# Kernel optimization log

Measured on AMD Instinct MI355X. Metric: run time of the kernel, lower is better.

Reference implementation:

```python
import jax, jax.numpy as jnp
import numpy as np

N, G, H1, H2, HEADS, EMB, C, S = 4096, 2048, 512, 128, 8, 16, 20, 4
CH = H1 // HEADS  # per-head channels = 64
EPS = 1e-6
COEF_FE = 0.1


def _uni(k, shape, fan_in, fan_out):
    c = np.sqrt(6.0 / (fan_in + fan_out)).astype(np.float32)
    return jax.random.uniform(k, shape, jnp.float32, -c, c)


def setup_inputs() -> dict:
    key = jax.random.key(0)
    ks = jax.random.split(key, 40)
    adj = (jax.random.uniform(ks[0], (N, N)) < 0.005).astype(jnp.float32)
    adj = jnp.maximum(adj, jnp.eye(N, dtype=jnp.float32))  # self-loops, no empty rows
    node_feats = jax.random.normal(ks[1], (N, G), jnp.float32)
    count_matrix = jax.random.randint(ks[2], (N, G), 0, 50).astype(jnp.float32)
    library_size = jax.random.uniform(ks[3], (N, 1), jnp.float32, 0.5, 2.0)
    slice_label = jax.random.randint(ks[4], (N,), 0, S)
    basis = jax.random.uniform(ks[5], (C, G), jnp.float32)
    # encoder GAT layer1: HEADS heads, c_in=G -> c_out=CH each
    We1 = _uni(ks[6], (HEADS, CH, G), G, CH)
    be1 = jnp.zeros((HEADS, CH), jnp.float32)
    v0e1 = _uni(ks[7], (HEADS, CH, 1), CH, 1)
    v1e1 = _uni(ks[8], (HEADS, CH, 1), CH, 1)
    # encoder dense layer2: H1 -> H2
    W2 = _uni(ks[9], (H2, H1), H1, H2)
    b2 = jnp.zeros((H2,), jnp.float32)
    # decoder GAT layer1: c_in = H2+EMB -> CH per head
    CIN_D = H2 + EMB
    Wd1 = _uni(ks[10], (HEADS, CH, CIN_D), CIN_D, CH)
    bd1 = jnp.zeros((HEADS, CH), jnp.float32)
    v0d1 = _uni(ks[11], (HEADS, CH, 1), CH, 1)
    v1d1 = _uni(ks[12], (HEADS, CH, 1), CH, 1)
    # decoder dense layer2: H1 -> G
    Wd2 = _uni(ks[13], (G, H1), H1, G)
    bd2 = jnp.zeros((G,), jnp.float32)
    # deconv alpha (H2+EMB -> 1) and beta (H2 -> C); zero-init in torch, small random here
    Wa = 0.01 * jax.random.normal(ks[14], (1, CIN_D), jnp.float32)
    ba = jnp.zeros((1,), jnp.float32)
    Wb = 0.01 * jax.random.normal(ks[15], (C, H2), jnp.float32)
    bb = jnp.zeros((C,), jnp.float32)
    gamma = 0.01 * jax.random.normal(ks[16], (S, G), jnp.float32)
    logtheta = 5.0 * jnp.ones((S, G), jnp.float32)
    emb_table = jax.random.normal(ks[17], (S, EMB), jnp.float32)
    return dict(adj_matrix=adj, node_feats=node_feats, count_matrix=count_matrix,
                library_size=library_size, slice_label=slice_label, basis=basis,
                We1=We1, be1=be1, v0e1=v0e1, v1e1=v1e1, W2=W2, b2=b2,
                Wd1=Wd1, bd1=bd1, v0d1=v0d1, v1d1=v1d1, Wd2=Wd2, bd2=bd2,
                Wa=Wa, ba=ba, Wb=Wb, bb=bb, gamma=gamma, logtheta=logtheta,
                emb_table=emb_table)


def _gat_head(x, adj, W, b, v0, v1):
    h = x @ W.T + b                       # [N, CH]
    logits = adj * ((h @ v0) + (h @ v1).T)  # [N, N]; zero where adj==0
    s = jax.nn.sigmoid(logits) - 0.5       # unnormalized attentions
    mask = adj != 0.0
    e = jnp.where(mask, jnp.exp(s), 0.0)    # sparse softmax over structural nonzeros (temp=1)
    den = e.sum(axis=1, keepdims=True)
    p = e / jnp.where(den == 0.0, 1.0, den)
    return p @ h                            # [N, CH]


def _gat_multi(x, adj, Ws, bs, v0s, v1s):
    return jnp.concatenate([_gat_head(x, adj, Ws[i], bs[i], v0s[i], v1s[i])
                            for i in range(HEADS)], axis=1)


def reference(adj_matrix, node_feats, count_matrix, library_size, slice_label, basis,
              We1, be1, v0e1, v1e1, W2, b2, Wd1, bd1, v0d1, v1d1, Wd2, bd2,
              Wa, ba, Wb, bb, gamma, logtheta, emb_table):
    # encoder
    H = jax.nn.elu(_gat_multi(node_feats, adj_matrix, We1, be1, v0e1, v1e1))
    Z = H @ W2.T + b2                                   # [N, H2]
    emb = emb_table[slice_label]                        # [N, EMB]
    # deconvolutioner
    beta = jax.nn.softmax(jax.nn.elu(Z) @ Wb.T + bb, axis=1)   # [N, C]
    Hc = jax.nn.elu(jnp.concatenate([Z, emb], axis=1))
    alpha = Hc @ Wa.T + ba                              # [N, 1]
    # decoder
    Hd = jax.nn.elu(_gat_multi(jnp.concatenate([Z, emb], axis=1), adj_matrix,
                               Wd1, bd1, v0d1, v1d1))
    X_recon = Hd @ Wd2.T + bd2                          # [N, G]
    features_loss = jnp.mean(jnp.sqrt(jnp.sum((node_feats - X_recon) ** 2, axis=1)))
    # NB deconvolution loss
    log_lam = jnp.log(beta @ basis + EPS) + alpha + gamma[slice_label]
    lam = jnp.exp(log_lam)
    th = jnp.exp(logtheta)[slice_label]                 # [N, G]
    mu = library_size * lam
    ll = (jax.lax.lgamma(count_matrix + th + EPS) - jax.lax.lgamma(th + EPS)
          + th * jnp.log(th + EPS) - th * jnp.log(th + mu + EPS)
          + count_matrix * jnp.log(mu + EPS) - count_matrix * jnp.log(th + mu + EPS))
    decon_loss = -jnp.mean(jnp.sum(ll, axis=1))
    return decon_loss + COEF_FE * features_loss
```

## Files before the change

### kernel.cpp

```cpp
#include <hip/hip_runtime.h>
#include <hip/hip_bf16.h>
#include <math.h>

#define N 4096
#define G 2048
#define H1 512
#define H2 128
#define HEADS 8
#define EMB 16
#define C 20
#define S 4
#define CH 64
#define CIN_D (H2 + EMB)
#define KD_PAD 160
#define KB_PAD 32
#define CAP 128
#define EPSV 1e-6f

typedef __attribute__((ext_vector_type(8))) short short8;
typedef __attribute__((ext_vector_type(8))) short bf16x8;
typedef __attribute__((ext_vector_type(4))) float f32x4;

__device__ __forceinline__ unsigned short f2b(float x) {
    __hip_bfloat16 h = __float2bfloat16(x);
    return *reinterpret_cast<unsigned short*>(&h);
}
__device__ __forceinline__ float b2f(unsigned short u) {
    unsigned int x = ((unsigned int)u) << 16;
    return __uint_as_float(x);
}
__device__ __forceinline__ float lgamma_fast(float x) {
    float sh = 0.f;
    while (x < 8.f) { sh -= __logf(x); x += 1.f; }
    float ix = 1.f / x;
    float lx = __logf(x);
    return (x - 0.5f) * lx - x + 0.91893853f
         + ix * (0.08333333f - 0.00277778f * ix * ix) + sh;
}

__global__ void build_csr(const float* __restrict__ adj, int* __restrict__ col_idx,
                          int* __restrict__ row_cnt) {
    int i = blockIdx.x;
    int lane = threadIdx.x;
    int cnt = 0;
    const float4* row4 = (const float4*)(adj + (size_t)i * N);
    int* cols = col_idx + (size_t)i * CAP;
    unsigned long long lmask = (1ull << lane) - 1ull;
    for (int c = 0; c < N / 256; ++c) {
        float4 v = row4[c * 64 + lane];
        float vv[4] = {v.x, v.y, v.z, v.w};
        #pragma unroll
        for (int s = 0; s < 4; ++s) {
            unsigned long long m = __ballot(vv[s] != 0.f);
            if (vv[s] != 0.f) {
                int idx = cnt + __popcll(m & lmask);
                if (idx < CAP) cols[idx] = c * 256 + lane * 4 + s;
            }
            cnt += __popcll(m);
        }
    }
    if (lane == 0) row_cnt[i] = cnt < CAP ? cnt : CAP;
}

#define SEG_SG   (S * G)
#define SEG_NF4  (N * G / 4)
#define SEG_WE4  (H1 * G / 4)
#define SEG_W24  (H2 * H1 / 4)
#define SEG_WD1E (H1 * KD_PAD)
#define SEG_WD24 (G * H1 / 4)
#define SEG_BTE  (G * KB_PAD)
#define PREP_TOTAL (SEG_SG + SEG_NF4 + SEG_WE4 + SEG_W24 + SEG_WD1E + SEG_WD24 + SEG_BTE)

__device__ __forceinline__ void cvt4(const float* __restrict__ in,
                                     unsigned short* __restrict__ out, int i) {
    float4 v = ((const float4*)in)[i];
    ushort4 o;
    o.x = f2b(v.x); o.y = f2b(v.y); o.z = f2b(v.z); o.w = f2b(v.w);
    ((ushort4*)out)[i] = o;
}

__global__ __launch_bounds__(256) void prep(const float* __restrict__ logtheta,
                                            const float* __restrict__ gamma,
                                            float* __restrict__ th_a, float* __restrict__ eg_a,
                                            float* __restrict__ gm_a, float* __restrict__ ax_a,
                                            const float* __restrict__ node_f,
                                            unsigned short* __restrict__ nf_bf,
                                            const float* __restrict__ We1,
                                            unsigned short* __restrict__ We1_bf,
                                            const float* __restrict__ W2,
                                            unsigned short* __restrict__ W2_bf,
                                            const float* __restrict__ Wd1,
                                            unsigned short* __restrict__ Wd1_bf,
                                            const float* __restrict__ Wd2,
                                            unsigned short* __restrict__ Wd2_bf,
                                            const float* __restrict__ basis,
                                            unsigned short* __restrict__ basisT_bf) {
    int idx = blockIdx.x * 256 + threadIdx.x;
    if (idx < SEG_SG) {
        float th = __expf(logtheta[idx]);
        float gm = gamma[idx];
        th_a[idx] = th;
        eg_a[idx] = __expf(gm);
        gm_a[idx] = gm;
        ax_a[idx] = th * __logf(th + EPSV) - lgammaf(th + EPSV);
        return;
    }
    idx -= SEG_SG;
    if (idx < SEG_NF4) { cvt4(node_f, nf_bf, idx); return; }
    idx -= SEG_NF4;
    if (idx < SEG_WE4) { cvt4(We1, We1_bf, idx); return; }
    idx -= SEG_WE4;
    if (idx < SEG_W24) { cvt4(W2, W2_bf, idx); return; }
    idx -= SEG_W24;
    if (idx < SEG_WD1E) {
        int n = idx / KD_PAD, k = idx - n * KD_PAD;
        Wd1_bf[idx] = f2b(k < CIN_D ? Wd1[n * CIN_D + k] : 0.f);
        return;
    }
    idx -= SEG_WD1E;
    if (idx < SEG_WD24) { cvt4(Wd2, Wd2_bf, idx); return; }
    idx -= SEG_WD24;
    if (idx < SEG_BTE) {
        int g = idx >> 5, c = idx & 31;
        basisT_bf[idx] = f2b(c < C ? basis[c * G + g] : 0.f);
    }
}

#define LDP 40
template<int FM, int OBF, int KS, int HV>
__global__ __launch_bounds__(256) void gemm_mfma(const unsigned short* __restrict__ A,
                                                 const unsigned short* __restrict__ B,
                                                 const float* __restrict__ bias,
                                                 void* __restrict__ Cout,
                                                 int M, int Nc, int K,
                                                 const float* __restrict__ v0f,
                                                 const float* __restrict__ v1f,
                                                 float* __restrict__ hv0,
                                                 float* __restrict__ hv1) {
    constexpr int BMT = FM * 32;
    __shared__ short As[BMT * LDP];
    __shared__ short Bs[128 * LDP];
    int bn = blockIdx.x, bm = blockIdx.y;
    int kz = (KS > 1) ? blockIdx.z : 0;
    int t = threadIdx.x;
    int lane = t & 63, wid = t >> 6;
    int wr = wid >> 1, wc = wid & 1;
    f32x4 acc[FM][4] = {};
    const short* Ag = (const short*)A + (size_t)(bm * BMT) * K;
    const short* Bg = (const short*)B + (size_t)(bn * 128) * K;
    int r0 = t >> 2, q0 = t & 3;
    int rbase = (lane & 15);
    int koff = (lane >> 4) * 8;
    int kbeg = kz * (K / KS), kend = kbeg + K / KS;

    for (int k0 = kbeg; k0 < kend; k0 += 32) {
        short8 a0 = *(const short8*)(Ag + (size_t)r0 * K + k0 + q0 * 8);
        short8 a1;
        if constexpr (FM == 4) a1 = *(const short8*)(Ag + (size_t)(r0 + 64) * K + k0 + q0 * 8);
        short8 b0 = *(const short8*)(Bg + (size_t)r0 * K + k0 + q0 * 8);
        short8 b1 = *(const short8*)(Bg + (size_t)(r0 + 64) * K + k0 + q0 * 8);
        __syncthreads();
        *(short8*)(As + r0 * LDP + q0 * 8) = a0;
        if constexpr (FM == 4) *(short8*)(As + (r0 + 64) * LDP + q0 * 8) = a1;
        *(short8*)(Bs + r0 * LDP + q0 * 8) = b0;
        *(short8*)(Bs + (r0 + 64) * LDP + q0 * 8) = b1;
        __syncthreads();
        bf16x8 af[FM], bfr[4];
        #pragma unroll
        for (int m = 0; m < FM; ++m)
            af[m] = *(const bf16x8*)(As + (wr * FM * 16 + m * 16 + rbase) * LDP + koff);
        #pragma unroll
        for (int n = 0; n < 4; ++n)
            bfr[n] = *(const bf16x8*)(Bs + (wc * 64 + n * 16 + rbase) * LDP + koff);
        #pragma unroll
        for (int m = 0; m < FM; ++m)
            #pragma unroll
            for (int n = 0; n < 4; ++n)
                acc[m][n] = __builtin_amdgcn_mfma_f32_16x16x32_bf16(af[m], bfr[n], acc[m][n], 0, 0, 0);
    }
    int colb = bn * 128 + wc * 64;
    int rowb = bm * BMT + wr * FM * 16;
    #pragma unroll
    for (int m = 0; m < FM; ++m) {
        #pragma unroll
        for (int n = 0; n < 4; ++n) {
            int col = colb + n * 16 + (lane & 15);
            int row0 = rowb + m * 16 + (lane >> 4) * 4;
            if constexpr (KS > 1) {
                float* Cp = (float*)Cout + (size_t)kz * M * Nc;
                #pragma unroll
                for (int r = 0; r < 4; ++r)
                    Cp[(size_t)(row0 + r) * Nc + col] = acc[m][n][r];
            } else {
                float bs = bias ? bias[col] : 0.f;
                #pragma unroll
                for (int r = 0; r < 4; ++r) {
                    float v = acc[m][n][r] + bs;
                    if constexpr (OBF)
                        ((unsigned short*)Cout)[(size_t)(row0 + r) * Nc + col] = f2b(v);
                    else
                        ((float*)Cout)[(size_t)(row0 + r) * Nc + col] = v;
                }
            }
        }
    }
    if constexpr (HV) {
        int h = colb >> 6;
        #pragma unroll
        for (int m = 0; m < FM; ++m) {
            #pragma unroll
            for (int r = 0; r < 4; ++r) {
                int row = rowb + m * 16 + (lane >> 4) * 4 + r;
                float p0 = 0.f, p1 = 0.f;
                #pragma unroll
                for (int n = 0; n < 4; ++n) {
                    int col = colb + n * 16 + (lane & 15);
                    float v = acc[m][n][r] + bias[col];
                    p0 += v * v0f[col];
                    p1 += v * v1f[col];
                }
                p0 += __shfl_xor(p0, 1); p0 += __shfl_xor(p0, 2);
                p0 += __shfl_xor(p0, 4); p0 += __shfl_xor(p0, 8);
                p1 += __shfl_xor(p1, 1); p1 += __shfl_xor(p1, 2);
                p1 += __shfl_xor(p1, 4); p1 += __shfl_xor(p1, 8);
                if ((lane & 15) == 0) {
                    hv0[row * HEADS + h] = p0;
                    hv1[row * HEADS + h] = p1;
                }
            }
        }
    }
}

template<int KS>
__global__ __launch_bounds__(256) void reduce_k(const float* __restrict__ Cp,
                                                const float* __restrict__ bias,
                                                float* __restrict__ out,
                                                int total4, int ncmask) {
    int i = blockIdx.x * 256 + threadIdx.x;
    if (i >= total4) return;
    float4 s = ((const float4*)Cp)[i];
    #pragma unroll
    for (int ks = 1; ks < KS; ++ks) {
        float4 v = ((const float4*)(Cp + (size_t)ks * total4 * 4))[i];
        s.x += v.x; s.y += v.y; s.z += v.z; s.w += v.w;
    }
    int col = (i * 4) & ncmask;
    s.x += bias[col]; s.y += bias[col + 1]; s.z += bias[col + 2]; s.w += bias[col + 3];
    ((float4*)out)[i] = s;
}

template<int KS>
__global__ __launch_bounds__(256) void reduce_k_hv(const float* __restrict__ Cp,
                                                   const float* __restrict__ bias,
                                                   unsigned short* __restrict__ out,
                                                   const float* __restrict__ v0f,
                                                   const float* __restrict__ v1f,
                                                   float* __restrict__ hv0,
                                                   float* __restrict__ hv1) {
    constexpr int total4 = N * H1 / 4;
    int t = threadIdx.x;
    int i = blockIdx.x * 256 + t;
    float4 s = ((const float4*)Cp)[i];
    #pragma unroll
    for (int ks = 1; ks < KS; ++ks) {
        float4 v = ((const float4*)(Cp + (size_t)ks * total4 * 4))[i];
        s.x += v.x; s.y += v.y; s.z += v.z; s.w += v.w;
    }
    int col = (i * 4) & (H1 - 1);
    s.x += bias[col]; s.y += bias[col + 1]; s.z += bias[col + 2]; s.w += bias[col + 3];
    ushort4 o;
    o.x = f2b(s.x); o.y = f2b(s.y); o.z = f2b(s.z); o.w = f2b(s.w);
    ((ushort4*)out)[i] = o;
    int row = (i * 4) >> 9;
    int h = col >> 6;
    float4 w0 = *(const float4*)(v0f + col);
    float4 w1 = *(const float4*)(v1f + col);
    float p0 = s.x * w0.x + s.y * w0.y + s.z * w0.z + s.w * w0.w;
    float p1 = s.x * w1.x + s.y * w1.y + s.z * w1.z + s.w * w1.w;
    p0 += __shfl_xor(p0, 1); p0 += __shfl_xor(p0, 2);
    p0 += __shfl_xor(p0, 4); p0 += __shfl_xor(p0, 8);
    p1 += __shfl_xor(p1, 1); p1 += __shfl_xor(p1, 2);
    p1 += __shfl_xor(p1, 4); p1 += __shfl_xor(p1, 8);
    if ((t & 15) == 0) {
        hv0[row * HEADS + h] = p0;
        hv1[row * HEADS + h] = p1;
    }
}

__global__ __launch_bounds__(256) void gemm_recon_sq(const unsigned short* __restrict__ A,
                                                     const unsigned short* __restrict__ B,
                                                     const float* __restrict__ bias,
                                                     const unsigned short* __restrict__ nfb,
                                                     float* __restrict__ sq_part) {
    constexpr int K = H1;
    __shared__ short As[64 * LDP];
    __shared__ short Bs[128 * LDP];
    __shared__ float red[4][32];
    int bn = blockIdx.x, bm = blockIdx.y;
    int t = threadIdx.x;
    int lane = t & 63, wid = t >> 6;
    int wr = wid >> 1, wc = wid & 1;
    f32x4 acc[2][4] = {};
    const short* Ag = (const short*)A + (size_t)(bm * 64) * K;
    const short* Bg = (const short*)B + (size_t)(bn * 128) * K;
    int r0 = t >> 2, q0 = t & 3;
    int rbase = (lane & 15);
    int koff = (lane >> 4) * 8;

    for (int k0 = 0; k0 < K; k0 += 32) {
        short8 a0 = *(const short8*)(Ag + (size_t)r0 * K + k0 + q0 * 8);
        short8 b0 = *(const short8*)(Bg + (size_t)r0 * K + k0 + q0 * 8);
        short8 b1 = *(const short8*)(Bg + (size_t)(r0 + 64) * K + k0 + q0 * 8);
        __syncthreads();
        *(short8*)(As + r0 * LDP + q0 * 8) = a0;
        *(short8*)(Bs + r0 * LDP + q0 * 8) = b0;
        *(short8*)(Bs + (r0 + 64) * LDP + q0 * 8) = b1;
        __syncthreads();
        bf16x8 af[2], bfr[4];
        #pragma unroll
        for (int m = 0; m < 2; ++m)
            af[m] = *(const bf16x8*)(As + (wr * 32 + m * 16 + rbase) * LDP + koff);
        #pragma unroll
        for (int n = 0; n < 4; ++n)
            bfr[n] = *(const bf16x8*)(Bs + (wc * 64 + n * 16 + rbase) * LDP + koff);
        #pragma unroll
        for (int m = 0; m < 2; ++m)
            #pragma unroll
            for (int n = 0; n < 4; ++n)
                acc[m][n] = __builtin_amdgcn_mfma_f32_16x16x32_bf16(af[m], bfr[n], acc[m][n], 0, 0, 0);
    }
    int colb = bn * 128 + wc * 64;
    int rowb = bm * 64 + wr * 32;
    float part[2][4];
    #pragma unroll
    for (int m = 0; m < 2; ++m) {
        #pragma unroll
        for (int r = 0; r < 4; ++r) part[m][r] = 0.f;
        #pragma unroll
        for (int n = 0; n < 4; ++n) {
            int col = colb + n * 16 + (lane & 15);
            float bs = bias[col];
            int row0 = rowb + m * 16 + (lane >> 4) * 4;
            #pragma unroll
            for (int r = 0; r < 4; ++r) {
                float d = b2f(nfb[(size_t)(row0 + r) * G + col]) - (acc[m][n][r] + bs);
                part[m][r] += d * d;
            }
        }
    }
    #pragma unroll
    for (int m = 0; m < 2; ++m)
        #pragma unroll
        for (int r = 0; r < 4; ++r) {
            float v = part[m][r];
            v += __shfl_xor(v, 1); v += __shfl_xor(v, 2);
            v += __shfl_xor(v, 4); v += __shfl_xor(v, 8);
            part[m][r] = v;
        }
    if ((lane & 15) == 0) {
        int q = lane >> 4;
        #pragma unroll
        for (int m = 0; m < 2; ++m)
            #pragma unroll
            for (int r = 0; r < 4; ++r)
                red[wid][m * 16 + q * 4 + r] = part[m][r];
    }
    __syncthreads();
    if (t < 64) {
        int wr2 = t >> 5, loc = t & 31;
        float v = red[wr2 * 2 + 0][loc] + red[wr2 * 2 + 1][loc];
        sq_part[(size_t)(bm * 64 + t) * 16 + bn] = v;
    }
}

__global__ __launch_bounds__(256) void bd_ll(const unsigned short* __restrict__ A,
                                             const unsigned short* __restrict__ B,
                                             const float* __restrict__ cm,
                                             const int* __restrict__ slab,
                                             const float* __restrict__ muf,
                                             const float* __restrict__ kco,
                                             const float* __restrict__ th_a,
                                             const float* __restrict__ eg_a,
                                             const float* __restrict__ gm_a,
                                             const float* __restrict__ ax_a,
                                             float* __restrict__ ll_part) {
    __shared__ short As[32 * LDP];
    __shared__ short Bs[128 * LDP];
    __shared__ float red[4][16];
    int bn = blockIdx.x, bm = blockIdx.y;
    int t = threadIdx.x;
    int lane = t & 63, wid = t >> 6;
    int wr = wid >> 1, wc = wid & 1;
    f32x4 acc[4] = {};
    const short* Ag = (const short*)A + (size_t)(bm * 32) * KB_PAD;
    const short* Bg = (const short*)B + (size_t)(bn * 128) * KB_PAD;
    int r0 = t >> 2, q0 = t & 3;
    if (t < 128) {
        short8 a0 = *(const short8*)(Ag + (size_t)r0 * KB_PAD + q0 * 8);
        *(short8*)(As + r0 * LDP + q0 * 8) = a0;
    }
    {
        short8 b0 = *(const short8*)(Bg + (size_t)r0 * KB_PAD + q0 * 8);
        short8 b1 = *(const short8*)(Bg + (size_t)(r0 + 64) * KB_PAD + q0 * 8);
        *(short8*)(Bs + r0 * LDP + q0 * 8) = b0;
        *(short8*)(Bs + (r0 + 64) * LDP + q0 * 8) = b1;
    }
    __syncthreads();
    int rbase = (lane & 15);
    int koff = (lane >> 4) * 8;
    bf16x8 af = *(const bf16x8*)(As + (wr * 16 + rbase) * LDP + koff);
    bf16x8 bfr[4];
    #pragma unroll
    for (int n = 0; n < 4; ++n)
        bfr[n] = *(const bf16x8*)(Bs + (wc * 64 + n * 16 + rbase) * LDP + koff);
    #pragma unroll
    for (int n = 0; n < 4; ++n)
        acc[n] = __builtin_amdgcn_mfma_f32_16x16x32_bf16(af, bfr[n], acc[n], 0, 0, 0);
    int colb = bn * 128 + wc * 64;
    int rowb = bm * 32 + wr * 16;
    #pragma unroll
    for (int r = 0; r < 4; ++r) {
        int row = rowb + (lane >> 4) * 4 + r;
        int sl = slab[row];
        float mufv = muf[row], kcov = kco[row];
        size_t sgb = (size_t)sl * G;
        float p = 0.f;
        #pragma unroll
        for (int n = 0; n < 4; ++n) {
            int col = colb + n * 16 + (lane & 15);
            float ebd = acc[n][r] + EPSV;
            float k = cm[(size_t)row * G + col];
            float th = th_a[sgb + col];
            float lbd = __logf(ebd);
            float mu = mufv * ebd * eg_a[sgb + col];
            float lgx = lgamma_fast(k + th + EPSV);
            p += lgx + ax_a[sgb + col] - (th + k) * __logf(th + mu + EPSV)
               + k * (kcov + lbd + gm_a[sgb + col]);
        }
        p += __shfl_xor(p, 1); p += __shfl_xor(p, 2);
        p += __shfl_xor(p, 4); p += __shfl_xor(p, 8);
        if ((lane & 15) == 0) red[wid][(lane >> 4) * 4 + r] = p;
    }
    __syncthreads();
    if (t < 32) {
        int wr2 = t >> 4, rl = t & 15;
        float v = red[wr2 * 2 + 0][rl] + red[wr2 * 2 + 1][rl];
        ll_part[(size_t)(bm * 32 + wr2 * 16 + rl) * 16 + bn] = v;
    }
}

__global__ __launch_bounds__(512) void attn_fused(const unsigned short* __restrict__ Hb,
                                                  const float* __restrict__ hv0,
                                                  const float* __restrict__ hv1,
                                                  const int* __restrict__ col_idx,
                                                  const int* __restrict__ row_cnt,
                                                  unsigned short* __restrict__ out) {
    __shared__ int scols[CAP];
    __shared__ float sw[CAP][HEADS];
    __shared__ float sden[HEADS];
    __shared__ float red[8][64 * 8];
    int i = blockIdx.x;
    int t = threadIdx.x;
    int cnt = row_cnt[i];
    const int* cols = col_idx + (size_t)i * CAP;
    if (t < cnt) scols[t] = cols[t];
    __syncthreads();
    for (int idx = t; idx < cnt * HEADS; idx += 512) {
        int e = idx >> 3, h = idx & 7;
        int j = scols[e];
        float x = hv0[i * HEADS + h] + hv1[j * HEADS + h];
        sw[e][h] = __expf(1.f / (1.f + __expf(-x)) - 0.5f);
    }
    __syncthreads();
    if (t < HEADS) {
        float d = 0.f;
        for (int e = 0; e < cnt; ++e) d += sw[e][t];
        sden[t] = 1.f / d;
    }
    __syncthreads();
    int slot = t >> 6;
    int cg = t & 63;
    int h = cg >> 3;
    float inv = sden[h];
    float acc[8];
    #pragma unroll
    for (int k = 0; k < 8; ++k) acc[k] = 0.f;
    for (int e = slot; e < cnt; e += 8) {
        int j = scols[e];
        float wv = sw[e][h] * inv;
        short8 hv = ((const short8*)(Hb + (size_t)j * H1))[cg];
        #pragma unroll
        for (int k = 0; k < 8; ++k)
            acc[k] += wv * b2f((unsigned short)hv[k]);
    }
    #pragma unroll
    for (int k = 0; k < 8; ++k) red[slot][cg * 8 + k] = acc[k];
    __syncthreads();
    if (slot < 4) {
        #pragma unroll
        for (int k = 0; k < 8; ++k) red[slot][cg * 8 + k] += red[slot + 4][cg * 8 + k];
    }
    __syncthreads();
    if (slot < 2) {
        #pragma unroll
        for (int k = 0; k < 8; ++k) red[slot][cg * 8 + k] += red[slot + 2][cg * 8 + k];
    }
    __syncthreads();
    if (slot == 0) {
        short8 o;
        #pragma unroll
        for (int k = 0; k < 8; ++k) {
            float v = red[0][cg * 8 + k] + red[1][cg * 8 + k];
            v = (v > 0.f) ? v : expm1f(v);
            o[k] = (short)f2b(v);
        }
        ((short8*)(out + (size_t)i * H1))[cg] = o;
    }
}

__global__ void pernode(const float* __restrict__ Z, const float* __restrict__ emb_table,
                        const int* __restrict__ slab, const float* __restrict__ Wb,
                        const float* __restrict__ bb, const float* __restrict__ Wa,
                        const float* __restrict__ ba, const float* __restrict__ lib,
                        unsigned short* __restrict__ beta_bf, float* __restrict__ muf,
                        float* __restrict__ kco, unsigned short* __restrict__ Xdb) {
    int i = blockIdx.x;
    int lane = threadIdx.x;
    __shared__ float sZ[H2];
    __shared__ float sE[EMB];
    __shared__ float sLog[C];
    __shared__ float sAl;
    sZ[lane] = Z[(size_t)i * H2 + lane];
    sZ[64 + lane] = Z[(size_t)i * H2 + 64 + lane];
    int s = slab[i];
    if (lane < EMB) sE[lane] = emb_table[s * EMB + lane];
    __syncthreads();
    Xdb[(size_t)i * KD_PAD + lane] = f2b(sZ[lane]);
    Xdb[(size_t)i * KD_PAD + 64 + lane] = f2b(sZ[64 + lane]);
    if (lane < EMB) Xdb[(size_t)i * KD_PAD + H2 + lane] = f2b(sE[lane]);
    if (lane < KD_PAD - CIN_D) Xdb[(size_t)i * KD_PAD + CIN_D + lane] = 0;
    if (lane < C) {
        float acc = bb[lane];
        for (int k = 0; k < H2; ++k) {
            float z = sZ[k];
            float e = z > 0.f ? z : expm1f(z);
            acc += e * Wb[lane * H2 + k];
        }
        sLog[lane] = acc;
    }
    __syncthreads();
    if (lane == 0) {
        float mx = sLog[0];
        for (int c = 1; c < C; ++c) mx = fmaxf(mx, sLog[c]);
        float sm = 0.f;
        for (int c = 0; c < C; ++c) { float e = __expf(sLog[c] - mx); sLog[c] = e; sm += e; }
        for (int c = 0; c < C; ++c) sLog[c] /= sm;
    }
    __syncthreads();
    if (lane < KB_PAD) beta_bf[(size_t)i * KB_PAD + lane] = (lane < C) ? f2b(sLog[lane]) : 0;
    float x0 = sZ[lane];        x0 = x0 > 0.f ? x0 : expm1f(x0);
    float x1 = sZ[64 + lane];   x1 = x1 > 0.f ? x1 : expm1f(x1);
    float p = x0 * Wa[lane] + x1 * Wa[64 + lane];
    if (lane < EMB) {
        float x2 = sE[lane];    x2 = x2 > 0.f ? x2 : expm1f(x2);
        p += x2 * Wa[H2 + lane];
    }
    #pragma unroll
    for (int m = 32; m; m >>= 1) p += __shfl_xor(p, m);
    if (lane == 0) sAl = p + ba[0];
    __syncthreads();
    if (lane == 0) {
        float A = sAl, L = lib[i];
        muf[i] = L * __expf(A);
        kco[i] = __logf(L) + A;
    }
}

__global__ void row_reduce(const float* __restrict__ ll_part, const float* __restrict__ sq_part,
                           float* __restrict__ part_ll, float* __restrict__ part_sq) {
    int blk = blockIdx.x, lane = threadIdx.x;
    int row = blk * 64 + lane;
    float s1 = 0.f, s2 = 0.f;
    #pragma unroll
    for (int j = 0; j < 16; ++j) {
        s1 += ll_part[(size_t)row * 16 + j];
        s2 += sq_part[(size_t)row * 16 + j];
    }
    float b = sqrtf(s2);
    #pragma unroll
    for (int m = 32; m; m >>= 1) { s1 += __shfl_xor(s1, m); b += __shfl_xor(b, m); }
    if (lane == 0) { part_ll[blk] = s1; part_sq[blk] = b; }
}

__global__ void finalize2(const float* __restrict__ part_ll, const float* __restrict__ part_sq,
                          float* __restrict__ out) {
    int lane = threadIdx.x;
    float a = part_ll[lane], b = part_sq[lane];
    #pragma unroll
    for (int m = 32; m; m >>= 1) { a += __shfl_xor(a, m); b += __shfl_xor(b, m); }
    if (lane == 0) out[0] = -(a / (float)N) + 0.1f * (b / (float)N);
}

extern "C" void kernel_launch(void* const* d_in, const int* in_sizes, int n_in,
                              void* d_out, int out_size, void* d_ws, size_t ws_size,
                              hipStream_t stream) {
    const float* adj       = (const float*)d_in[0];
    const float* node_f    = (const float*)d_in[1];
    const float* count_m   = (const float*)d_in[2];
    const float* lib       = (const float*)d_in[3];
    const int*   slab      = (const int*)d_in[4];
    const float* basis     = (const float*)d_in[5];
    const float* We1       = (const float*)d_in[6];
    const float* be1       = (const float*)d_in[7];
    const float* v0e1      = (const float*)d_in[8];
    const float* v1e1      = (const float*)d_in[9];
    const float* W2        = (const float*)d_in[10];
    const float* b2        = (const float*)d_in[11];
    const float* Wd1       = (const float*)d_in[12];
    const float* bd1       = (const float*)d_in[13];
    const float* v0d1      = (const float*)d_in[14];
    const float* v1d1      = (const float*)d_in[15];
    const float* Wd2       = (const float*)d_in[16];
    const float* bd2       = (const float*)d_in[17];
    const float* Wa        = (const float*)d_in[18];
    const float* ba        = (const float*)d_in[19];
    const float* Wb        = (const float*)d_in[20];
    const float* bb        = (const float*)d_in[21];
    const float* gamma     = (const float*)d_in[22];
    const float* logtheta  = (const float*)d_in[23];
    const float* emb_table = (const float*)d_in[24];
    float* out = (float*)d_out;

    char* w = (char*)d_ws;
    auto alloc = [&](size_t bytes) { void* p = (void*)w; w += (bytes + 255) & ~(size_t)255; return p; };
    int*   col_idx = (int*)  alloc((size_t)N * CAP * 4);
    int*   row_cnt = (int*)  alloc((size_t)N * 4);
    unsigned short* Hlin_bf = (unsigned short*)alloc((size_t)N * H1 * 2);
    unsigned short* Hgat_bf = (unsigned short*)alloc((size_t)N * H1 * 2);
    float* Z       = (float*)alloc((size_t)N * H2 * 4);
    unsigned short* Xd_bf   = (unsigned short*)alloc((size_t)N * KD_PAD * 2);
    unsigned short* beta_bf = (unsigned short*)alloc((size_t)N * KB_PAD * 2);
    float* muf     = (float*)alloc((size_t)N * 4);
    float* kco     = (float*)alloc((size_t)N * 4);
    float* hv0     = (float*)alloc((size_t)N * HEADS * 4);
    float* hv1     = (float*)alloc((size_t)N * HEADS * 4);
    float* th_a    = (float*)alloc((size_t)S * G * 4);
    float* eg_a    = (float*)alloc((size_t)S * G * 4);
    float* gm_a    = (float*)alloc((size_t)S * G * 4);
    float* ax_a    = (float*)alloc((size_t)S * G * 4);
    float* Cp      = (float*)alloc((size_t)4 * N * H1 * 4);
    float* ll_part = (float*)alloc((size_t)N * 16 * 4);
    float* sq_part = (float*)alloc((size_t)N * 16 * 4);
    float* part_ll = (float*)alloc(64 * 4);
    float* part_sq = (float*)alloc(64 * 4);
    unsigned short* nf_bf    = (unsigned short*)alloc((size_t)N * G * 2);
    unsigned short* We1_bf   = (unsigned short*)alloc((size_t)H1 * G * 2);
    unsigned short* W2_bf    = (unsigned short*)alloc((size_t)H2 * H1 * 2);
    unsigned short* Wd1_bf   = (unsigned short*)alloc((size_t)H1 * KD_PAD * 2);
    unsigned short* Wd2_bf   = (unsigned short*)alloc((size_t)G * H1 * 2);
    unsigned short* basisT_bf= (unsigned short*)alloc((size_t)G * KB_PAD * 2);

    build_csr<<<dim3(N), dim3(64), 0, stream>>>(adj, col_idx, row_cnt);
    prep<<<dim3(PREP_TOTAL / 256), dim3(256), 0, stream>>>(
        logtheta, gamma, th_a, eg_a, gm_a, ax_a,
        node_f, nf_bf, We1, We1_bf, W2, W2_bf, Wd1, Wd1_bf, Wd2, Wd2_bf, basis, basisT_bf);

    gemm_mfma<2, 0, 4, 0><<<dim3(H1 / 128, N / 64, 4), dim3(256), 0, stream>>>(
        nf_bf, We1_bf, be1, Cp, N, H1, G, nullptr, nullptr, nullptr, nullptr);
    reduce_k_hv<4><<<dim3(N * H1 / 4 / 256), dim3(256), 0, stream>>>(
        Cp, be1, Hlin_bf, v0e1, v1e1, hv0, hv1);
    attn_fused<<<dim3(N), dim3(512), 0, stream>>>(Hlin_bf, hv0, hv1, col_idx, row_cnt, Hgat_bf);
    gemm_mfma<2, 0, 8, 0><<<dim3(H2 / 128, N / 64, 8), dim3(256), 0, stream>>>(
        Hgat_bf, W2_bf, b2, Cp, N, H2, H1, nullptr, nullptr, nullptr, nullptr);
    reduce_k<8><<<dim3((N * H2 / 4 + 255) / 256), dim3(256), 0, stream>>>(
        Cp, b2, Z, N * H2 / 4, H2 - 1);
    pernode<<<dim3(N), dim3(64), 0, stream>>>(Z, emb_table, slab, Wb, bb, Wa, ba, lib,
                                              beta_bf, muf, kco, Xd_bf);
    bd_ll<<<dim3(G / 128, N / 32), dim3(256), 0, stream>>>(
        beta_bf, basisT_bf, count_m, slab, muf, kco, th_a, eg_a, gm_a, ax_a, ll_part);
    gemm_mfma<2, 1, 1, 1><<<dim3(H1 / 128, N / 64), dim3(256), 0, stream>>>(
        Xd_bf, Wd1_bf, bd1, Hlin_bf, N, H1, KD_PAD, v0d1, v1d1, hv0, hv1);
    attn_fused<<<dim3(N), dim3(512), 0, stream>>>(Hlin_bf, hv0, hv1, col_idx, row_cnt, Hgat_bf);
    gemm_recon_sq<<<dim3(G / 128, N / 64), dim3(256), 0, stream>>>(
        Hgat_bf, Wd2_bf, bd2, nf_bf, sq_part);
    row_reduce<<<dim3(64), dim3(64), 0, stream>>>(ll_part, sq_part, part_ll, part_sq);
    finalize2<<<dim3(1), dim3(64), 0, stream>>>(part_ll, part_sq, out);
}
```

Before: 186.1 us.

## Split fused beta@basis GEMM and NB loss into GEMM plus row-wise elementwise kernel

Replaces the fused bd_ll kernel, which computed beta@basis via MFMA and evaluated the negative-binomial log-likelihood in the MFMA output layout, with two steps. The first is a generic gemm_mfma that writes beta@basis to a bf16 N×G buffer. The second is a row-per-wavefront elementwise kernel that reads it with vectorized coalesced loads and reduces each row directly. The aim is coalesced access to count_matrix and the per-slice tables and no cross-block partial sums. The cost is an extra 16 MB write and read of the intermediate and one more kernel launch.

```diff
diff --git a/kernel.cpp b/kernel.cpp
--- a/kernel.cpp
+++ b/kernel.cpp
@@ -374,80 +374,48 @@
     }
 }
 
-__global__ __launch_bounds__(256) void bd_ll(const unsigned short* __restrict__ A,
-                                             const unsigned short* __restrict__ B,
-                                             const float* __restrict__ cm,
-                                             const int* __restrict__ slab,
-                                             const float* __restrict__ muf,
-                                             const float* __restrict__ kco,
-                                             const float* __restrict__ th_a,
-                                             const float* __restrict__ eg_a,
-                                             const float* __restrict__ gm_a,
-                                             const float* __restrict__ ax_a,
-                                             float* __restrict__ ll_part) {
-    __shared__ short As[32 * LDP];
-    __shared__ short Bs[128 * LDP];
-    __shared__ float red[4][16];
-    int bn = blockIdx.x, bm = blockIdx.y;
-    int t = threadIdx.x;
-    int lane = t & 63, wid = t >> 6;
-    int wr = wid >> 1, wc = wid & 1;
-    f32x4 acc[4] = {};
-    const short* Ag = (const short*)A + (size_t)(bm * 32) * KB_PAD;
-    const short* Bg = (const short*)B + (size_t)(bn * 128) * KB_PAD;
-    int r0 = t >> 2, q0 = t & 3;
-    if (t < 128) {
-        short8 a0 = *(const short8*)(Ag + (size_t)r0 * KB_PAD + q0 * 8);
-        *(short8*)(As + r0 * LDP + q0 * 8) = a0;
-    }
-    {
-        short8 b0 = *(const short8*)(Bg + (size_t)r0 * KB_PAD + q0 * 8);
-        short8 b1 = *(const short8*)(Bg + (size_t)(r0 + 64) * KB_PAD + q0 * 8);
-        *(short8*)(Bs + r0 * LDP + q0 * 8) = b0;
-        *(short8*)(Bs + (r0 + 64) * LDP + q0 * 8) = b1;
-    }
-    __syncthreads();
-    int rbase = (lane & 15);
-    int koff = (lane >> 4) * 8;
-    bf16x8 af = *(const bf16x8*)(As + (wr * 16 + rbase) * LDP + koff);
-    bf16x8 bfr[4];
-    #pragma unroll
-    for (int n = 0; n < 4; ++n)
-        bfr[n] = *(const bf16x8*)(Bs + (wc * 64 + n * 16 + rbase) * LDP + koff);
-    #pragma unroll
-    for (int n = 0; n < 4; ++n)
-        acc[n] = __builtin_amdgcn_mfma_f32_16x16x32_bf16(af, bfr[n], acc[n], 0, 0, 0);
-    int colb = bn * 128 + wc * 64;
-    int rowb = bm * 32 + wr * 16;
-    #pragma unroll
-    for (int r = 0; r < 4; ++r) {
-        int row = rowb + (lane >> 4) * 4 + r;
-        int sl = slab[row];
-        float mufv = muf[row], kcov = kco[row];
-        size_t sgb = (size_t)sl * G;
-        float p = 0.f;
-        #pragma unroll
-        for (int n = 0; n < 4; ++n) {
-            int col = colb + n * 16 + (lane & 15);
-            float ebd = acc[n][r] + EPSV;
-            float k = cm[(size_t)row * G + col];
-            float th = th_a[sgb + col];
+__global__ __launch_bounds__(256) void nb_loss_ew(const unsigned short* __restrict__ BDb,
+                                                  const float* __restrict__ cm,
+                                                  const int* __restrict__ slab,
+                                                  const float* __restrict__ muf,
+                                                  const float* __restrict__ kco,
+                                                  const float* __restrict__ th_a,
+                                                  const float* __restrict__ eg_a,
+                                                  const float* __restrict__ gm_a,
+                                                  const float* __restrict__ ax_a,
+                                                  float* __restrict__ ll_row) {
+    int row = blockIdx.x * 4 + (threadIdx.x >> 6);
+    int lane = threadIdx.x & 63;
+    int sl = slab[row];
+    float mufv = muf[row], kcov = kco[row];
+    const unsigned short* bdr = BDb + (size_t)row * G;
+    const float* cmr = cm + (size_t)row * G;
+    size_t sgb = (size_t)sl * G;
+    float acc = 0.f;
+    #pragma unroll 2
+    for (int it = 0; it < G / 256; ++it) {
+        int c = it * 256 + lane * 4;
+        ushort4 bdu = *(const ushort4*)(bdr + c);
+        f32x4 k4  = *(const f32x4*)(cmr + c);
+        f32x4 th4 = *(const f32x4*)(th_a + sgb + c);
+        f32x4 eg4 = *(const f32x4*)(eg_a + sgb + c);
+        f32x4 gm4 = *(const f32x4*)(gm_a + sgb + c);
+        f32x4 ax4 = *(const f32x4*)(ax_a + sgb + c);
+        float bdv[4] = {b2f(bdu.x), b2f(bdu.y), b2f(bdu.z), b2f(bdu.w)};
+        #pragma unroll
+        for (int j = 0; j < 4; ++j) {
+            float th = th4[j], k = k4[j];
+            float ebd = bdv[j] + EPSV;
             float lbd = __logf(ebd);
-            float mu = mufv * ebd * eg_a[sgb + col];
+            float mu = mufv * ebd * eg4[j];
             float lgx = lgamma_fast(k + th + EPSV);
-            p += lgx + ax_a[sgb + col] - (th + k) * __logf(th + mu + EPSV)
-               + k * (kcov + lbd + gm_a[sgb + col]);
-        }
-        p += __shfl_xor(p, 1); p += __shfl_xor(p, 2);
-        p += __shfl_xor(p, 4); p += __shfl_xor(p, 8);
-        if ((lane & 15) == 0) red[wid][(lane >> 4) * 4 + r] = p;
-    }
-    __syncthreads();
-    if (t < 32) {
-        int wr2 = t >> 4, rl = t & 15;
-        float v = red[wr2 * 2 + 0][rl] + red[wr2 * 2 + 1][rl];
-        ll_part[(size_t)(bm * 32 + wr2 * 16 + rl) * 16 + bn] = v;
-    }
+            acc += lgx + ax4[j] - (th + k) * __logf(th + mu + EPSV)
+                 + k * (kcov + lbd + gm4[j]);
+        }
+    }
+    #pragma unroll
+    for (int m = 32; m; m >>= 1) acc += __shfl_xor(acc, m);
+    if (lane == 0) ll_row[row] = acc;
 }
 
 __global__ __launch_bounds__(512) void attn_fused(const unsigned short* __restrict__ Hb,
@@ -577,16 +545,14 @@
     }
 }
 
-__global__ void row_reduce(const float* __restrict__ ll_part, const float* __restrict__ sq_part,
+__global__ void row_reduce(const float* __restrict__ ll_row, const float* __restrict__ sq_part,
                            float* __restrict__ part_ll, float* __restrict__ part_sq) {
     int blk = blockIdx.x, lane = threadIdx.x;
     int row = blk * 64 + lane;
-    float s1 = 0.f, s2 = 0.f;
-    #pragma unroll
-    for (int j = 0; j < 16; ++j) {
-        s1 += ll_part[(size_t)row * 16 + j];
-        s2 += sq_part[(size_t)row * 16 + j];
-    }
+    float s1 = ll_row[row];
+    float s2 = 0.f;
+    #pragma unroll
+    for (int j = 0; j < 16; ++j) s2 += sq_part[(size_t)row * 16 + j];
     float b = sqrtf(s2);
     #pragma unroll
     for (int m = 32; m; m >>= 1) { s1 += __shfl_xor(s1, m); b += __shfl_xor(b, m); }
@@ -650,7 +616,8 @@
     float* gm_a    = (float*)alloc((size_t)S * G * 4);
     float* ax_a    = (float*)alloc((size_t)S * G * 4);
     float* Cp      = (float*)alloc((size_t)4 * N * H1 * 4);
-    float* ll_part = (float*)alloc((size_t)N * 16 * 4);
+    unsigned short* BDb = (unsigned short*)alloc((size_t)N * G * 2);
+    float* ll_row  = (float*)alloc((size_t)N * 4);
     float* sq_part = (float*)alloc((size_t)N * 16 * 4);
     float* part_ll = (float*)alloc(64 * 4);
     float* part_sq = (float*)alloc(64 * 4);
@@ -677,13 +644,15 @@
         Cp, b2, Z, N * H2 / 4, H2 - 1);
     pernode<<<dim3(N), dim3(64), 0, stream>>>(Z, emb_table, slab, Wb, bb, Wa, ba, lib,
                                               beta_bf, muf, kco, Xd_bf);
-    bd_ll<<<dim3(G / 128, N / 32), dim3(256), 0, stream>>>(
-        beta_bf, basisT_bf, count_m, slab, muf, kco, th_a, eg_a, gm_a, ax_a, ll_part);
+    gemm_mfma<2, 1, 1, 0><<<dim3(G / 128, N / 64), dim3(256), 0, stream>>>(
+        beta_bf, basisT_bf, nullptr, BDb, N, G, KB_PAD, nullptr, nullptr, nullptr, nullptr);
+    nb_loss_ew<<<dim3(N / 4), dim3(256), 0, stream>>>(
+        BDb, count_m, slab, muf, kco, th_a, eg_a, gm_a, ax_a, ll_row);
     gemm_mfma<2, 1, 1, 1><<<dim3(H1 / 128, N / 64), dim3(256), 0, stream>>>(
         Xd_bf, Wd1_bf, bd1, Hlin_bf, N, H1, KD_PAD, v0d1, v1d1, hv0, hv1);
     attn_fused<<<dim3(N), dim3(512), 0, stream>>>(Hlin_bf, hv0, hv1, col_idx, row_cnt, Hgat_bf);
     gemm_recon_sq<<<dim3(G / 128, N / 64), dim3(256), 0, stream>>>(
         Hgat_bf, Wd2_bf, bd2, nf_bf, sq_part);
-    row_reduce<<<dim3(64), dim3(64), 0, stream>>>(ll_part, sq_part, part_ll, part_sq);
+    row_reduce<<<dim3(64), dim3(64), 0, stream>>>(ll_row, sq_part, part_ll, part_sq);
     finalize2<<<dim3(1), dim3(64), 0, stream>>>(part_ll, part_sq, out);
 }
```

New measurement: 190.5 us. 2.4% more time.
